# Performance work log

Measured on AMD Instinct MI355X. Metric: run time of the kernel, lower is better.

The kernel has to match this reference:

```python
import jax, jax.numpy as jnp
import numpy as np

DIM = 96
HID = 384
DEPTH = 5
HEADS = 8
INNER = 64 * DIM          # inner_dim = dim_head * dim per source (dim_head=64)
DH = INNER // HEADS       # per-head dim = 768
SCALE = 64 ** -0.5        # scale uses default dim_head=64, not actual per-head dim
EPS = 1e-5


def setup_inputs() -> dict:
    key = jax.random.key(0)
    ks = jax.random.split(key, 13)
    def p(k, shape, s=0.02):
        return jax.random.normal(k, shape, jnp.float32) * s
    return {
        "x": jax.random.normal(ks[0], (2, 512, DIM), jnp.float32),
        "gam_a": p(ks[1], (DEPTH, 3, DIM)),          # attention pre-norm gammas
        "Wq": p(ks[2], (DEPTH, 3, DIM, INNER)),
        "Wk": p(ks[3], (DEPTH, 3, DIM, INNER)),
        "Wv": p(ks[4], (DEPTH, 3, DIM, INNER)),
        "Wo": p(ks[5], (DEPTH, 3, INNER, DIM)),
        "gam_m": p(ks[6], (DEPTH, 2, DIM)),          # MLP pre-norm gammas
        "W1": p(ks[7], (DEPTH, 2, DIM, HID)),
        "b1": p(ks[8], (DEPTH, 2, HID)),
        "W2": p(ks[9], (DEPTH, 2, HID, DIM)),
        "b2": p(ks[10], (DEPTH, 2, DIM)),
        "gam_mid": p(ks[11], (DEPTH, DIM)),          # bare LayerNorm inside each block
        "gam_final": p(ks[12], (DIM,)),
    }


def _ln(x, g):
    # nn.LayerNorm(elementwise_affine=False) followed by x * (gamma + 1)
    mu = x.mean(-1, keepdims=True)
    var = ((x - mu) ** 2).mean(-1, keepdims=True)
    return (x - mu) * jax.lax.rsqrt(var + EPS) * (g + 1.0)


def _attn(x, g, wq, wk, wv, wo):
    b, n, _ = x.shape
    h = _ln(x, g)                                    # self.norm (reuse_attention=True)
    q = (h @ wq).reshape(b, n, HEADS, DH).transpose(0, 2, 1, 3) * SCALE
    k = (h @ wk).reshape(b, n, HEADS, DH).transpose(0, 2, 1, 3)
    v = (h @ wv).reshape(b, n, HEADS, DH).transpose(0, 2, 1, 3)
    sim = jnp.einsum("bhid,bhjd->bhij", q, k)        # [b,h,n,n]
    a = jax.nn.softmax(sim, axis=-1)                 # dropout=0.0 -> identity
    o = jnp.einsum("bhij,bhjd->bhid", a, v)
    return o.transpose(0, 2, 1, 3).reshape(b, n, INNER) @ wo


def _mlp(x, g, w1, b1_, w2, b2_):
    # LayerNorm -> Linear -> GELU(exact) -> Linear (dropouts eval-mode identity)
    h = jax.nn.gelu(_ln(x, g) @ w1 + b1_, approximate=False)
    return h @ w2 + b2_


def reference(x, gam_a, Wq, Wk, Wv, Wo, gam_m, W1, b1, W2, b2, gam_mid, gam_final):
    for d in range(DEPTH):
        x = _attn(x, gam_a[d, 0], Wq[d, 0], Wk[d, 0], Wv[d, 0], Wo[d, 0]) + x
        x = _mlp(x, gam_m[d, 0], W1[d, 0], b1[d, 0], W2[d, 0], b2[d, 0]) + x
        x = _attn(x, gam_a[d, 1], Wq[d, 1], Wk[d, 1], Wv[d, 1], Wo[d, 1]) + x
        x = _attn(x, gam_a[d, 2], Wq[d, 2], Wk[d, 2], Wv[d, 2], Wo[d, 2]) + x
        x = _ln(x, gam_mid[d])                       # bare LayerNorm, NO residual
        x = _mlp(x, gam_m[d, 1], W1[d, 1], b1[d, 1], W2[d, 1], b2[d, 1]) + x
    return _ln(x, gam_final)
```

## Files before the change

### kernel.cpp

```cpp
#include <hip/hip_runtime.h>
#include <hip/hip_bf16.h>

typedef __hip_bfloat16 bf16;
typedef __attribute__((ext_vector_type(8))) short bf16x8;
typedef __attribute__((ext_vector_type(4))) float f32x4;

#define TOK    1024
#define DIM    96
#define HIDN   384
#define HEADS  8
#define DH     768
#define INNER  6144
#define SEQ    512
#define NDEPTH 5
#define EPSLN  1e-5f
#define QSCALE 0.125f

#define MFMA16(a, b, c) __builtin_amdgcn_mfma_f32_16x16x32_bf16((a), (b), (c), 0, 0, 0)

__device__ __forceinline__ float b2f(bf16 v) { return __bfloat162float(v); }
__device__ __forceinline__ bf16  f2b(float v) { return __float2bfloat16(v); }

__device__ __forceinline__ float gload(const void* p, size_t i, int f) {
  return f ? b2f(((const bf16*)p)[i]) : ((const float*)p)[i];
}
__device__ __forceinline__ const char* gptr(const void* base, size_t off, int f) {
  return (const char*)base + off * (size_t)(f ? 2 : 4);
}

__device__ __forceinline__ uint4 pack8(float4 u0, float4 u1) {
  alignas(16) unsigned short o[8];
  bf16 t;
  t = f2b(u0.x); o[0] = *(unsigned short*)&t;
  t = f2b(u0.y); o[1] = *(unsigned short*)&t;
  t = f2b(u0.z); o[2] = *(unsigned short*)&t;
  t = f2b(u0.w); o[3] = *(unsigned short*)&t;
  t = f2b(u1.x); o[4] = *(unsigned short*)&t;
  t = f2b(u1.y); o[5] = *(unsigned short*)&t;
  t = f2b(u1.z); o[6] = *(unsigned short*)&t;
  t = f2b(u1.w); o[7] = *(unsigned short*)&t;
  return *(const uint4*)o;
}

__global__ __launch_bounds__(256) void detect_kernel(const void* xraw, int* flag) {
  __shared__ int cnt[256];
  int t = threadIdx.x;
  const unsigned short* u = (const unsigned short*)xraw;
  int c = 0;
  #pragma unroll
  for (int i = 0; i < 4; i++) {
    unsigned short h = u[2 * (t * 4 + i)];
    int e = (h >> 7) & 0xFF;
    if (e >= 87 && e <= 132) c++;
  }
  cnt[t] = c;
  __syncthreads();
  for (int s = 128; s > 0; s >>= 1) {
    if (t < s) cnt[t] += cnt[t + s];
    __syncthreads();
  }
  if (t == 0) *flag = (cnt[0] > 700) ? 1 : 0;
}

__global__ __launch_bounds__(256) void wtrans_all_kernel(
    const void* __restrict__ Wo, const void* __restrict__ W1,
    const void* __restrict__ W2, bf16* __restrict__ woT,
    bf16* __restrict__ w1T, bf16* __restrict__ w2T,
    const int* __restrict__ flagp) {
  __shared__ float tile[32][65];
  int f = *flagp;
  int b = blockIdx.x;
  const void* src; bf16* dst; int R, C, bx, by, bz;
  if (b < 5760) {
    src = Wo; dst = woT; R = INNER; C = DIM;
    bz = b / 384; int rem = b % 384; bx = rem & 1; by = rem >> 1;
  } else if (b < 5940) {
    int idx = b - 5760;
    src = W1; dst = w1T; R = DIM; C = HIDN;
    bx = idx % 6; by = (idx / 6) % 3; bz = idx / 18;
  } else {
    int idx = b - 5940;
    src = W2; dst = w2T; R = HIDN; C = DIM;
    bx = idx & 1; by = (idx >> 1) % 12; bz = idx / 24;
  }
  int t = threadIdx.x;
  int c0 = bx * 64, r0 = by * 32;
  size_t bb = (size_t)bz * R * C;
  int ty = t >> 4, tx = t & 15;
  #pragma unroll
  for (int half = 0; half < 2; half++) {
    int r = r0 + ty + half * 16;
    int c = c0 + tx * 4;
    if (c < C) {
      size_t idx = bb + (size_t)r * C + c;
      float v0, v1, v2, v3;
      if (f) {
        uint2 u = *(const uint2*)((const unsigned short*)src + idx);
        v0 = __uint_as_float((u.x & 0xffffu) << 16);
        v1 = __uint_as_float(u.x & 0xffff0000u);
        v2 = __uint_as_float((u.y & 0xffffu) << 16);
        v3 = __uint_as_float(u.y & 0xffff0000u);
      } else {
        float4 v = *(const float4*)((const float*)src + idx);
        v0 = v.x; v1 = v.y; v2 = v.z; v3 = v.w;
      }
      tile[ty + half * 16][tx * 4 + 0] = v0;
      tile[ty + half * 16][tx * 4 + 1] = v1;
      tile[ty + half * 16][tx * 4 + 2] = v2;
      tile[ty + half * 16][tx * 4 + 3] = v3;
    }
  }
  __syncthreads();
  int cc = c0 + (t >> 2), rseg = (t & 3) * 8;
  if (cc < C) {
    int cs = cc - c0;
    alignas(16) unsigned short o[8];
    #pragma unroll
    for (int j = 0; j < 8; j++) {
      bf16 tv = f2b(tile[rseg + j][cs]);
      o[j] = *(unsigned short*)&tv;
    }
    *(uint4*)&dst[bb + (size_t)cc * R + r0 + rseg] = *(const uint4*)o;
  }
}

template <int WM>
__device__ __forceinline__ void gemm_bt_body(
    const void* __restrict__ A, int aF32, int lda,
    const void* __restrict__ Bt, int bF32, int ldb,
    int m0, int n0, int kbeg, int kend, int Mtot, int N,
    float alpha, bf16* __restrict__ Cb, float* __restrict__ Cf, int ldc) {
  constexpr int TM = WM * 32;
  __shared__ bf16 As[TM][40];
  __shared__ bf16 Bs[128][40];
  int t = threadIdx.x;
  int lane = t & 63;
  int wave = t >> 6;
  int wm = (wave >> 1) * (WM * 16), wn = (wave & 1) * 64;
  f32x4 acc[WM][4];
  #pragma unroll
  for (int i = 0; i < WM; i++)
    #pragma unroll
    for (int j = 0; j < 4; j++) acc[i][j] = (f32x4){0.f, 0.f, 0.f, 0.f};

  int arow = t >> 2, aseg = (t & 3) * 8;

  for (int kb = kbeg; kb < kend; kb += 32) {
    #pragma unroll
    for (int i = 0; i < (TM + 63) / 64; i++) {
      int rr = arow + i * 64;
      if ((TM % 64 == 0) || rr < TM) {
        int gm = min(m0 + rr, Mtot - 1);
        size_t idx = (size_t)gm * lda + kb + aseg;
        if (aF32) {
          const float* Af = (const float*)A;
          float4 u0 = *(const float4*)(Af + idx);
          float4 u1 = *(const float4*)(Af + idx + 4);
          *(uint4*)&As[rr][aseg] = pack8(u0, u1);
        } else {
          *(uint4*)&As[rr][aseg] = *(const uint4*)((const bf16*)A + idx);
        }
      }
    }
    #pragma unroll
    for (int i = 0; i < 2; i++) {
      int r = arow + i * 64;
      int gn = n0 + r;
      if (gn < N) {
        size_t idx = (size_t)gn * ldb + kb + aseg;
        if (bF32) {
          const float* Bf = (const float*)Bt;
          float4 u0 = *(const float4*)(Bf + idx);
          float4 u1 = *(const float4*)(Bf + idx + 4);
          *(uint4*)&Bs[r][aseg] = pack8(u0, u1);
        } else {
          *(uint4*)&Bs[r][aseg] = *(const uint4*)((const bf16*)Bt + idx);
        }
      } else {
        uint4 zz = {0, 0, 0, 0};
        *(uint4*)&Bs[r][aseg] = zz;
      }
    }
    __syncthreads();
    int fm = lane & 15, fq = (lane >> 4) * 8;
    bf16x8 af[WM], bfv[4];
    #pragma unroll
    for (int i = 0; i < WM; i++)
      af[i] = *(const bf16x8*)&As[wm + i * 16 + fm][fq];
    #pragma unroll
    for (int j = 0; j < 4; j++)
      bfv[j] = *(const bf16x8*)&Bs[wn + j * 16 + fm][fq];
    #pragma unroll
    for (int i = 0; i < WM; i++)
      #pragma unroll
      for (int j = 0; j < 4; j++)
        acc[i][j] = MFMA16(af[i], bfv[j], acc[i][j]);
    __syncthreads();
  }
  int col = lane & 15, rq = (lane >> 4) * 4;
  #pragma unroll
  for (int j = 0; j < 4; j++) {
    int gn = n0 + wn + j * 16 + col;
    if (gn >= N) continue;
    #pragma unroll
    for (int i = 0; i < WM; i++) {
      #pragma unroll
      for (int r = 0; r < 4; r++) {
        int gm = m0 + wm + i * 16 + rq + r;
        if (gm >= Mtot) continue;
        if (Cf) Cf[(size_t)gm * ldc + gn] = acc[i][j][r];
        else    Cb[(size_t)gm * ldc + gn] = f2b(acc[i][j][r] * alpha);
      }
    }
  }
}

__global__ __launch_bounds__(256) void mtgt_kernel(
    const void* __restrict__ WqE, const void* __restrict__ WkE,
    const void* __restrict__ WvE, const bf16* __restrict__ woT,
    float* __restrict__ P, const int* __restrict__ flagp) {
  int f = *flagp;
  int z = blockIdx.z;
  int ks = blockIdx.x / 3, mt = blockIdx.x % 3;
  bool isM = z < 120;
  int zz = isM ? z : z - 120;
  int L = zz >> 3, h = zz & 7;
  size_t wo = (size_t)L * DIM * INNER + (size_t)h * DH;
  const void* A  = isM ? (const void*)((const char*)WkE + wo * (f ? 2 : 4))
                       : (const void*)(woT + wo);
  const void* Bt = isM ? (const void*)((const char*)WqE + wo * (f ? 2 : 4))
                       : (const void*)((const char*)WvE + wo * (f ? 2 : 4));
  int aF32 = isM ? !f : 0;
  int bF32 = !f;
  float* Cf = P + ((size_t)ks * 240 + z) * DIM * DIM;
  gemm_bt_body<1>(A, aF32, INNER, Bt, bF32, INNER,
                  mt * 32, 0, ks * (DH / 4), (ks + 1) * (DH / 4), DIM, DIM,
                  1.f, nullptr, Cf, DIM);
}

__device__ __forceinline__ void ln_row_vals(float v0, float v1in, int lane,
    const char* g, int f, float& o0, float& o1) {
  float v1 = (lane < 32) ? v1in : 0.f;
  float s = v0 + v1;
  #pragma unroll
  for (int off = 32; off > 0; off >>= 1) s += __shfl_xor(s, off);
  float mu = s * (1.f / 96.f);
  float d0 = v0 - mu;
  float d1 = (lane < 32) ? (v1 - mu) : 0.f;
  float q = d0 * d0 + d1 * d1;
  #pragma unroll
  for (int off = 32; off > 0; off >>= 1) q += __shfl_xor(q, off);
  float rstd = rsqrtf(q * (1.f / 96.f) + EPSLN);
  o0 = d0 * rstd * (gload(g, lane, f) + 1.f);
  o1 = (lane < 32) ? (d1 * rstd * (gload(g, 64 + lane, f) + 1.f)) : 0.f;
}

__device__ __forceinline__ void store_hn(bf16* hn, bf16* hnT, int row, int lane,
                                         float o0, float o1) {
  size_t base = (size_t)row * DIM;
  bf16* hT = hnT + (size_t)(row >> 9) * DIM * SEQ;
  int ss = row & (SEQ - 1);
  hn[base + lane] = f2b(o0);
  hT[(size_t)lane * SEQ + ss] = f2b(o0);
  if (lane < 32) {
    hn[base + 64 + lane] = f2b(o1);
    hT[(size_t)(64 + lane) * SEQ + ss] = f2b(o1);
  }
}

__global__ __launch_bounds__(256) void cvtcast_kernel(
    const float* __restrict__ P, bf16* __restrict__ Mt, bf16* __restrict__ Gt,
    const void* __restrict__ in_x, float* __restrict__ x,
    bf16* __restrict__ hn, bf16* __restrict__ hnT,
    const void* __restrict__ gb, const int* __restrict__ flagp) {
  if (blockIdx.x < 2160) {
    const int n = 240 * DIM * DIM;
    int i0 = (blockIdx.x * 256 + threadIdx.x) * 4;
    if (i0 >= n) return;
    int z = i0 / (DIM * DIM);
    bool isM = z < 120;
    float alpha = isM ? QSCALE : 1.f;
    float4 a = *(const float4*)(P + i0);
    float4 b = *(const float4*)(P + n + i0);
    float4 c = *(const float4*)(P + 2 * (size_t)n + i0);
    float4 d = *(const float4*)(P + 3 * (size_t)n + i0);
    bf16* out = isM ? (Mt + i0) : (Gt + (size_t)i0 - (size_t)120 * DIM * DIM);
    alignas(8) unsigned short o[4];
    bf16 t;
    t = f2b(((a.x + b.x) + (c.x + d.x)) * alpha); o[0] = *(unsigned short*)&t;
    t = f2b(((a.y + b.y) + (c.y + d.y)) * alpha); o[1] = *(unsigned short*)&t;
    t = f2b(((a.z + b.z) + (c.z + d.z)) * alpha); o[2] = *(unsigned short*)&t;
    t = f2b(((a.w + b.w) + (c.w + d.w)) * alpha); o[3] = *(unsigned short*)&t;
    *(uint2*)out = *(const uint2*)o;
  } else {
    int f = *flagp;
    int wave = threadIdx.x >> 6, lane = threadIdx.x & 63;
    int row = (blockIdx.x - 2160) * 4 + wave;
    size_t base = (size_t)row * DIM;
    float v0 = gload(in_x, base + lane, f);
    float v1 = (lane < 32) ? gload(in_x, base + 64 + lane, f) : 0.f;
    x[base + lane] = v0;
    if (lane < 32) x[base + 64 + lane] = v1;
    float o0, o1;
    ln_row_vals(v0, v1, lane, gptr(gb, 0, f), f, o0, o1);
    store_hn(hn, hnT, row, lane, o0, o1);
  }
}

__global__ __launch_bounds__(256) void ln_kernel(
    const float* __restrict__ x, bf16* __restrict__ hn, bf16* __restrict__ hnT,
    const void* __restrict__ gb, size_t goff, const int* __restrict__ flagp) {
  int f = *flagp;
  int wave = threadIdx.x >> 6, lane = threadIdx.x & 63;
  int row = blockIdx.x * 4 + wave;
  size_t base = (size_t)row * DIM;
  float v0 = x[base + lane];
  float v1 = (lane < 32) ? x[base + 64 + lane] : 0.f;
  float o0, o1;
  ln_row_vals(v0, v1, lane, gptr(gb, goff, f), f, o0, o1);
  store_hn(hn, hnT, row, lane, o0, o1);
}

__global__ __launch_bounds__(512) void fattn4_kernel(
    const bf16* __restrict__ hn,
    const bf16* __restrict__ hnT,
    const bf16* __restrict__ MtL,
    const bf16* __restrict__ GtL,
    float* __restrict__ x) {
  __shared__ bf16 tP[32][520];
  __shared__ bf16 Zs[32][104];
  __shared__ float red[2][8][32];
  int tid = threadIdx.x, lane = tid & 63, wave = tid >> 6;
  int fm = lane & 15, fq = (lane >> 4) * 8;
  int col = lane & 15, rq = (lane >> 4) * 4;
  int z = blockIdx.y, b = z >> 3, h = z & 7;
  int m0 = blockIdx.x * 32;
  const bf16* hnB = hn + (size_t)b * SEQ * DIM;
  const bf16* hTB = hnT + (size_t)b * DIM * SEQ;
  const bf16* MtH = MtL + (size_t)h * DIM * DIM;
  const bf16* GtH = GtL + (size_t)h * DIM * DIM;

  if (wave < 6) {
    int mA = wave & 1, nb = wave >> 1;
    f32x4 a0 = (f32x4){0.f, 0.f, 0.f, 0.f}, a1 = a0;
    #pragma unroll
    for (int kb = 0; kb < 96; kb += 32) {
      bf16x8 af = *(const bf16x8*)(hnB + (size_t)(m0 + mA * 16 + fm) * DIM + kb + fq);
      bf16x8 b0 = *(const bf16x8*)(MtH + (size_t)(nb * 16 + fm) * DIM + kb + fq);
      bf16x8 b1 = *(const bf16x8*)(MtH + (size_t)((nb + 3) * 16 + fm) * DIM + kb + fq);
      a0 = MFMA16(af, b0, a0);
      a1 = MFMA16(af, b1, a1);
    }
    #pragma unroll
    for (int r = 0; r < 4; r++) {
      Zs[mA * 16 + rq + r][nb * 16 + col] = f2b(a0[r]);
      Zs[mA * 16 + rq + r][(nb + 3) * 16 + col] = f2b(a1[r]);
    }
  }
  __syncthreads();

  f32x4 acc2[2][4];
  #pragma unroll
  for (int i = 0; i < 2; i++)
    #pragma unroll
    for (int j = 0; j < 4; j++) acc2[i][j] = (f32x4){0.f, 0.f, 0.f, 0.f};
  #pragma unroll
  for (int kb = 0; kb < 96; kb += 32) {
    bf16x8 af0 = *(const bf16x8*)&Zs[fm][kb + fq];
    bf16x8 af1 = *(const bf16x8*)&Zs[16 + fm][kb + fq];
    bf16x8 bv[4];
    #pragma unroll
    for (int j = 0; j < 4; j++)
      bv[j] = *(const bf16x8*)(hnB + (size_t)(wave * 64 + j * 16 + fm) * DIM + kb + fq);
    #pragma unroll
    for (int j = 0; j < 4; j++) {
      acc2[0][j] = MFMA16(af0, bv[j], acc2[0][j]);
      acc2[1][j] = MFMA16(af1, bv[j], acc2[1][j]);
    }
  }

  float rmax[2][4];
  #pragma unroll
  for (int i = 0; i < 2; i++)
    #pragma unroll
    for (int r = 0; r < 4; r++) {
      float m = -1e30f;
      #pragma unroll
      for (int j = 0; j < 4; j++) m = fmaxf(m, acc2[i][j][r]);
      rmax[i][r] = m;
    }
  #pragma unroll
  for (int s = 1; s < 16; s <<= 1)
    #pragma unroll
    for (int i = 0; i < 2; i++)
      #pragma unroll
      for (int r = 0; r < 4; r++)
        rmax[i][r] = fmaxf(rmax[i][r], __shfl_xor(rmax[i][r], s));
  if (col == 0)
    #pragma unroll
    for (int i = 0; i < 2; i++)
      #pragma unroll
      for (int r = 0; r < 4; r++) red[0][wave][i * 16 + rq + r] = rmax[i][r];
  __syncthreads();
  float rsum[2][4];
  #pragma unroll
  for (int i = 0; i < 2; i++)
    #pragma unroll
    for (int r = 0; r < 4; r++) {
      int row = i * 16 + rq + r;
      float gm = red[0][0][row];
      #pragma unroll
      for (int q = 1; q < 8; q++) gm = fmaxf(gm, red[0][q][row]);
      float s = 0.f;
      #pragma unroll
      for (int j = 0; j < 4; j++) {
        float e = __expf(acc2[i][j][r] - gm);
        acc2[i][j][r] = e;
        s += e;
      }
      rsum[i][r] = s;
    }
  #pragma unroll
  for (int s = 1; s < 16; s <<= 1)
    #pragma unroll
    for (int i = 0; i < 2; i++)
      #pragma unroll
      for (int r = 0; r < 4; r++)
        rsum[i][r] += __shfl_xor(rsum[i][r], s);
  if (col == 0)
    #pragma unroll
    for (int i = 0; i < 2; i++)
      #pragma unroll
      for (int r = 0; r < 4; r++) red[1][wave][i * 16 + rq + r] = rsum[i][r];
  __syncthreads();

  #pragma unroll
  for (int i = 0; i < 2; i++)
    #pragma unroll
    for (int r = 0; r < 4; r++) {
      int row = i * 16 + rq + r;
      float tot = red[1][0][row];
      #pragma unroll
      for (int q = 1; q < 8; q++) tot += red[1][q][row];
      float inv = 1.f / tot;
      #pragma unroll
      for (int j = 0; j < 4; j++)
        tP[row][wave * 64 + j * 16 + col] = f2b(acc2[i][j][r] * inv);
    }
  __syncthreads();

  f32x4 z0 = (f32x4){0.f, 0.f, 0.f, 0.f}, z1 = z0;
  if (wave < 4) {
    int n = wave;
    #pragma unroll 4
    for (int kb = 0; kb < 512; kb += 32) {
      bf16x8 bv = *(const bf16x8*)(hTB + (size_t)(n * 16 + fm) * SEQ + kb + fq);
      bf16x8 af0 = *(const bf16x8*)&tP[fm][kb + fq];
      bf16x8 af1 = *(const bf16x8*)&tP[16 + fm][kb + fq];
      z0 = MFMA16(af0, bv, z0);
      z1 = MFMA16(af1, bv, z1);
    }
    #pragma unroll
    for (int r = 0; r < 4; r++) {
      Zs[rq + r][n * 16 + col] = f2b(z0[r]);
      Zs[16 + rq + r][n * 16 + col] = f2b(z1[r]);
    }
  } else {
    int mA = wave & 1, n = (wave >> 1) + 2;
    #pragma unroll 4
    for (int kb = 0; kb < 512; kb += 32) {
      bf16x8 bv = *(const bf16x8*)(hTB + (size_t)(n * 16 + fm) * SEQ + kb + fq);
      bf16x8 af = *(const bf16x8*)&tP[mA * 16 + fm][kb + fq];
      z0 = MFMA16(af, bv, z0);
    }
    #pragma unroll
    for (int r = 0; r < 4; r++)
      Zs[mA * 16 + rq + r][n * 16 + col] = f2b(z0[r]);
  }
  __syncthreads();

  if (wave < 6) {
    int mA = wave & 1, nb = wave >> 1;
    f32x4 o0 = (f32x4){0.f, 0.f, 0.f, 0.f}, o1 = o0;
    #pragma unroll
    for (int kb = 0; kb < 96; kb += 32) {
      bf16x8 af = *(const bf16x8*)&Zs[mA * 16 + fm][kb + fq];
      bf16x8 b0 = *(const bf16x8*)(GtH + (size_t)(nb * 16 + fm) * DIM + kb + fq);
      bf16x8 b1 = *(const bf16x8*)(GtH + (size_t)((nb + 3) * 16 + fm) * DIM + kb + fq);
      o0 = MFMA16(af, b0, o0);
      o1 = MFMA16(af, b1, o1);
    }
    #pragma unroll
    for (int r = 0; r < 4; r++) {
      int gr = b * SEQ + m0 + mA * 16 + rq + r;
      atomicAdd(x + (size_t)gr * DIM + nb * 16 + col, o0[r]);
      atomicAdd(x + (size_t)gr * DIM + (nb + 3) * 16 + col, o1[r]);
    }
  }
}

__global__ __launch_bounds__(512) void fmlp_kernel(
    float* __restrict__ X,
    const void* __restrict__ gmidb, size_t gmidoff, int useMid,
    const void* __restrict__ gmb, size_t gmoff,
    const bf16* __restrict__ w1T,
    const void* __restrict__ b1b, size_t b1off,
    const bf16* __restrict__ w2T,
    const void* __restrict__ b2b, size_t b2off,
    int lnmode, const void* __restrict__ lngb, size_t lngoff,
    bf16* __restrict__ hn, bf16* __restrict__ hnT, void* __restrict__ dout,
    const int* __restrict__ flagp) {
  __shared__ float X1s[32][96];
  __shared__ bf16 As[32][104];
  __shared__ bf16 Hs[32][392];
  int f = *flagp;
  int tid = threadIdx.x, lane = tid & 63, wave = tid >> 6;
  int fm = lane & 15, fq = (lane >> 4) * 8;
  int col = lane & 15, rq = (lane >> 4) * 4;
  int m0 = blockIdx.x * 32;
  const char* gm = gptr(gmb, gmoff, f);
  float gm0 = gload(gm, lane, f) + 1.f;
  float gm1 = (lane < 32) ? (gload(gm, 64 + lane, f) + 1.f) : 0.f;
  float gd0 = 1.f, gd1 = 1.f;
  if (useMid) {
    const char* gmid = gptr(gmidb, gmidoff, f);
    gd0 = gload(gmid, lane, f) + 1.f;
    gd1 = (lane < 32) ? (gload(gmid, 64 + lane, f) + 1.f) : 0.f;
  }
  for (int r = wave; r < 32; r += 8) {
    const float* xr = X + (size_t)(m0 + r) * DIM;
    float v0 = xr[lane];
    float v1 = (lane < 32) ? xr[64 + lane] : 0.f;
    if (useMid) {
      float s = v0 + v1;
      #pragma unroll
      for (int off = 32; off > 0; off >>= 1) s += __shfl_xor(s, off);
      float mu = s * (1.f / 96.f);
      float d0 = v0 - mu;
      float d1 = (lane < 32) ? (v1 - mu) : 0.f;
      float q = d0 * d0 + d1 * d1;
      #pragma unroll
      for (int off = 32; off > 0; off >>= 1) q += __shfl_xor(q, off);
      float rstd = rsqrtf(q * (1.f / 96.f) + EPSLN);
      v0 = d0 * rstd * gd0;
      v1 = (lane < 32) ? (d1 * rstd * gd1) : 0.f;
    }
    X1s[r][lane] = v0;
    if (lane < 32) X1s[r][64 + lane] = v1;
    float s = v0 + v1;
    #pragma unroll
    for (int off = 32; off > 0; off >>= 1) s += __shfl_xor(s, off);
    float mu = s * (1.f / 96.f);
    float d0 = v0 - mu;
    float d1 = (lane < 32) ? (v1 - mu) : 0.f;
    float q = d0 * d0 + d1 * d1;
    #pragma unroll
    for (int off = 32; off > 0; off >>= 1) q += __shfl_xor(q, off);
    float rstd = rsqrtf(q * (1.f / 96.f) + EPSLN);
    As[r][lane] = f2b(d0 * rstd * gm0);
    if (lane < 32) As[r][64 + lane] = f2b(d1 * rstd * gm1);
  }
  __syncthreads();

  int mw = wave & 1, nh = wave >> 1;
  f32x4 acc1[6];
  #pragma unroll
  for (int j = 0; j < 6; j++) acc1[j] = (f32x4){0.f, 0.f, 0.f, 0.f};
  #pragma unroll
  for (int kb = 0; kb < 96; kb += 32) {
    bf16x8 af = *(const bf16x8*)&As[mw * 16 + fm][kb + fq];
    #pragma unroll
    for (int j = 0; j < 6; j++) {
      bf16x8 bv = *(const bf16x8*)(w1T + (size_t)(nh * 96 + j * 16 + fm) * DIM + kb + fq);
      acc1[j] = MFMA16(af, bv, acc1[j]);
    }
  }
  const char* b1p = gptr(b1b, b1off, f);
  #pragma unroll
  for (int j = 0; j < 6; j++) {
    int gn = nh * 96 + j * 16 + col;
    float bv = gload(b1p, gn, f);
    #pragma unroll
    for (int r = 0; r < 4; r++) {
      float v = acc1[j][r] + bv;
      v = 0.5f * v * (1.f + erff(v * 0.70710678118f));
      Hs[mw * 16 + rq + r][gn] = f2b(v);
    }
  }
  __syncthreads();

  if (wave < 6) {
    int mA = wave & 1, nb = wave >> 1;
    f32x4 o0 = (f32x4){0.f, 0.f, 0.f, 0.f}, o1 = o0;
    #pragma unroll 4
    for (int kb = 0; kb < 384; kb += 32) {
      bf16x8 af = *(const bf16x8*)&Hs[mA * 16 + fm][kb + fq];
      bf16x8 b0 = *(const bf16x8*)(w2T + (size_t)(nb * 16 + fm) * HIDN + kb + fq);
      bf16x8 b1 = *(const bf16x8*)(w2T + (size_t)((nb + 3) * 16 + fm) * HIDN + kb + fq);
      o0 = MFMA16(af, b0, o0);
      o1 = MFMA16(af, b1, o1);
    }
    const char* b2p = gptr(b2b, b2off, f);
    float bb0 = gload(b2p, nb * 16 + col, f);
    float bb1 = gload(b2p, (nb + 3) * 16 + col, f);
    #pragma unroll
    for (int r = 0; r < 4; r++) {
      int row = mA * 16 + rq + r;
      int gmr = m0 + row;
      float nv0 = X1s[row][nb * 16 + col] + o0[r] + bb0;
      float nv1 = X1s[row][(nb + 3) * 16 + col] + o1[r] + bb1;
      X[(size_t)gmr * DIM + nb * 16 + col] = nv0;
      X[(size_t)gmr * DIM + (nb + 3) * 16 + col] = nv1;
      X1s[row][nb * 16 + col] = nv0;
      X1s[row][(nb + 3) * 16 + col] = nv1;
    }
  }
  __syncthreads();

  const char* lg = gptr(lngb, lngoff, f);
  for (int r = wave; r < 32; r += 8) {
    int row = m0 + r;
    size_t base = (size_t)row * DIM;
    float v0 = X1s[r][lane];
    float v1 = (lane < 32) ? X1s[r][64 + lane] : 0.f;
    float o0, o1;
    ln_row_vals(v0, v1, lane, lg, f, o0, o1);
    if (lnmode == 1) {
      store_hn(hn, hnT, row, lane, o0, o1);
    } else {
      if (!f) {
        ((float*)dout)[base + lane] = o0;
        if (lane < 32) ((float*)dout)[base + 64 + lane] = o1;
      } else {
        ((bf16*)dout)[base + lane] = f2b(o0);
        if (lane < 32) ((bf16*)dout)[base + 64 + lane] = f2b(o1);
      }
    }
  }
}

extern "C" void kernel_launch(void* const* d_in, const int* in_sizes, int n_in,
                              void* d_out, int out_size, void* d_ws, size_t ws_size,
                              hipStream_t stream) {
  const void* in_x    = d_in[0];
  const void* gam_a   = d_in[1];
  const void* Wq      = d_in[2];
  const void* Wk      = d_in[3];
  const void* Wv      = d_in[4];
  const void* Wo      = d_in[5];
  const void* gam_m   = d_in[6];
  const void* W1      = d_in[7];
  const void* b1      = d_in[8];
  const void* W2      = d_in[9];
  const void* b2      = d_in[10];
  const void* gam_mid = d_in[11];
  const void* gam_fin = d_in[12];

  char* wsb = (char*)d_ws;
  size_t off = 0;
  auto carve = [&](size_t bytes) {
    char* p = wsb + off;
    off += (bytes + 255) & ~(size_t)255;
    return p;
  };
  int*   flag = (int*)carve(256);
  float* x    = (float*)carve((size_t)TOK * DIM * 4);
  bf16*  hn   = (bf16*)carve((size_t)TOK * DIM * 2);
  bf16*  hnT  = (bf16*)carve((size_t)2 * DIM * SEQ * 2);
  const size_t WSZ = (size_t)15 * DIM * INNER;
  bf16*  woT  = (bf16*)carve(WSZ * 2);
  bf16*  w1T  = (bf16*)carve((size_t)10 * DIM * HIDN * 2);
  bf16*  w2T  = (bf16*)carve((size_t)10 * DIM * HIDN * 2);
  bf16*  Mt   = (bf16*)carve((size_t)120 * DIM * DIM * 2);
  bf16*  Gt   = (bf16*)carve((size_t)120 * DIM * DIM * 2);
  float* MtP  = (float*)carve((size_t)4 * 240 * DIM * DIM * 4);

  detect_kernel<<<dim3(1), dim3(256), 0, stream>>>(in_x, flag);

  wtrans_all_kernel<<<dim3(6180), dim3(256), 0, stream>>>(
      Wo, W1, W2, woT, w1T, w2T, flag);
  mtgt_kernel<<<dim3(12, 1, 240), dim3(256), 0, stream>>>(
      Wq, Wk, Wv, woT, MtP, flag);
  cvtcast_kernel<<<dim3(2160 + 256), dim3(256), 0, stream>>>(
      MtP, Mt, Gt, in_x, x, hn, hnT, gam_a, flag);

  auto attn = [&](int d, int j) {
    size_t gi = ((size_t)d * 3 + j);
    fattn4_kernel<<<dim3(16, 16), dim3(512), 0, stream>>>(
        hn, hnT, Mt + gi * 8 * DIM * DIM, Gt + gi * 8 * DIM * DIM, x);
  };

  for (int d = 0; d < NDEPTH; d++) {
    bool last = (d == NDEPTH - 1);
    attn(d, 0);
    fmlp_kernel<<<dim3(32), dim3(512), 0, stream>>>(
        x, nullptr, 0, 0,
        gam_m, (size_t)(d * 2 + 0) * DIM,
        w1T + (size_t)(d * 2 + 0) * DIM * HIDN, b1, (size_t)(d * 2 + 0) * HIDN,
        w2T + (size_t)(d * 2 + 0) * DIM * HIDN, b2, (size_t)(d * 2 + 0) * DIM,
        1, gam_a, (size_t)(d * 3 + 1) * DIM, hn, hnT, nullptr, flag);
    attn(d, 1);
    ln_kernel<<<dim3(TOK / 4), dim3(256), 0, stream>>>(
        x, hn, hnT, gam_a, (size_t)(d * 3 + 2) * DIM, flag);
    attn(d, 2);
    fmlp_kernel<<<dim3(32), dim3(512), 0, stream>>>(
        x, gam_mid, (size_t)d * DIM, 1,
        gam_m, (size_t)(d * 2 + 1) * DIM,
        w1T + (size_t)(d * 2 + 1) * DIM * HIDN, b1, (size_t)(d * 2 + 1) * HIDN,
        w2T + (size_t)(d * 2 + 1) * DIM * HIDN, b2, (size_t)(d * 2 + 1) * DIM,
        last ? 2 : 1, last ? gam_fin : gam_a,
        last ? (size_t)0 : (size_t)((d + 1) * 3) * DIM,
        hn, hnT, d_out, flag);
  }
}
```

Baseline: 662.3 us.

## Halve attention query tile to 16 rows and halve split-K in weight fold

```diff
diff --git a/kernel.cpp b/kernel.cpp
--- a/kernel.cpp
+++ b/kernel.cpp
@@ -234,7 +234,7 @@
   int bF32 = !f;
   float* Cf = P + ((size_t)ks * 240 + z) * DIM * DIM;
   gemm_bt_body<1>(A, aF32, INNER, Bt, bF32, INNER,
-                  mt * 32, 0, ks * (DH / 4), (ks + 1) * (DH / 4), DIM, DIM,
+                  mt * 32, 0, ks * (DH / 2), (ks + 1) * (DH / 2), DIM, DIM,
                   1.f, nullptr, Cf, DIM);
 }
 
@@ -282,15 +282,13 @@
     float alpha = isM ? QSCALE : 1.f;
     float4 a = *(const float4*)(P + i0);
     float4 b = *(const float4*)(P + n + i0);
-    float4 c = *(const float4*)(P + 2 * (size_t)n + i0);
-    float4 d = *(const float4*)(P + 3 * (size_t)n + i0);
     bf16* out = isM ? (Mt + i0) : (Gt + (size_t)i0 - (size_t)120 * DIM * DIM);
     alignas(8) unsigned short o[4];
     bf16 t;
-    t = f2b(((a.x + b.x) + (c.x + d.x)) * alpha); o[0] = *(unsigned short*)&t;
-    t = f2b(((a.y + b.y) + (c.y + d.y)) * alpha); o[1] = *(unsigned short*)&t;
-    t = f2b(((a.z + b.z) + (c.z + d.z)) * alpha); o[2] = *(unsigned short*)&t;
-    t = f2b(((a.w + b.w) + (c.w + d.w)) * alpha); o[3] = *(unsigned short*)&t;
+    t = f2b((a.x + b.x) * alpha); o[0] = *(unsigned short*)&t;
+    t = f2b((a.y + b.y) * alpha); o[1] = *(unsigned short*)&t;
+    t = f2b((a.z + b.z) * alpha); o[2] = *(unsigned short*)&t;
+    t = f2b((a.w + b.w) * alpha); o[3] = *(unsigned short*)&t;
     *(uint2*)out = *(const uint2*)o;
   } else {
     int f = *flagp;
@@ -321,180 +319,142 @@
   store_hn(hn, hnT, row, lane, o0, o1);
 }
 
-__global__ __launch_bounds__(512) void fattn4_kernel(
+__global__ __launch_bounds__(512) void fattn5_kernel(
     const bf16* __restrict__ hn,
     const bf16* __restrict__ hnT,
     const bf16* __restrict__ MtL,
     const bf16* __restrict__ GtL,
     float* __restrict__ x) {
-  __shared__ bf16 tP[32][520];
-  __shared__ bf16 Zs[32][104];
-  __shared__ float red[2][8][32];
+  __shared__ bf16 tP[16][520];
+  __shared__ bf16 Zs[16][104];
+  __shared__ float red[2][8][16];
   int tid = threadIdx.x, lane = tid & 63, wave = tid >> 6;
   int fm = lane & 15, fq = (lane >> 4) * 8;
   int col = lane & 15, rq = (lane >> 4) * 4;
   int z = blockIdx.y, b = z >> 3, h = z & 7;
-  int m0 = blockIdx.x * 32;
+  int m0 = blockIdx.x * 16;
   const bf16* hnB = hn + (size_t)b * SEQ * DIM;
   const bf16* hTB = hnT + (size_t)b * DIM * SEQ;
   const bf16* MtH = MtL + (size_t)h * DIM * DIM;
   const bf16* GtH = GtL + (size_t)h * DIM * DIM;
 
   if (wave < 6) {
-    int mA = wave & 1, nb = wave >> 1;
-    f32x4 a0 = (f32x4){0.f, 0.f, 0.f, 0.f}, a1 = a0;
+    int n = wave;
+    f32x4 a0 = (f32x4){0.f, 0.f, 0.f, 0.f};
     #pragma unroll
     for (int kb = 0; kb < 96; kb += 32) {
-      bf16x8 af = *(const bf16x8*)(hnB + (size_t)(m0 + mA * 16 + fm) * DIM + kb + fq);
-      bf16x8 b0 = *(const bf16x8*)(MtH + (size_t)(nb * 16 + fm) * DIM + kb + fq);
-      bf16x8 b1 = *(const bf16x8*)(MtH + (size_t)((nb + 3) * 16 + fm) * DIM + kb + fq);
-      a0 = MFMA16(af, b0, a0);
-      a1 = MFMA16(af, b1, a1);
-    }
-    #pragma unroll
-    for (int r = 0; r < 4; r++) {
-      Zs[mA * 16 + rq + r][nb * 16 + col] = f2b(a0[r]);
-      Zs[mA * 16 + rq + r][(nb + 3) * 16 + col] = f2b(a1[r]);
-    }
-  }
-  __syncthreads();
-
-  f32x4 acc2[2][4];
-  #pragma unroll
-  for (int i = 0; i < 2; i++)
-    #pragma unroll
-    for (int j = 0; j < 4; j++) acc2[i][j] = (f32x4){0.f, 0.f, 0.f, 0.f};
+      bf16x8 af = *(const bf16x8*)(hnB + (size_t)(m0 + fm) * DIM + kb + fq);
+      bf16x8 bv = *(const bf16x8*)(MtH + (size_t)(n * 16 + fm) * DIM + kb + fq);
+      a0 = MFMA16(af, bv, a0);
+    }
+    #pragma unroll
+    for (int r = 0; r < 4; r++)
+      Zs[rq + r][n * 16 + col] = f2b(a0[r]);
+  }
+  __syncthreads();
+
+  f32x4 acc2[4];
+  #pragma unroll
+  for (int j = 0; j < 4; j++) acc2[j] = (f32x4){0.f, 0.f, 0.f, 0.f};
   #pragma unroll
   for (int kb = 0; kb < 96; kb += 32) {
-    bf16x8 af0 = *(const bf16x8*)&Zs[fm][kb + fq];
-    bf16x8 af1 = *(const bf16x8*)&Zs[16 + fm][kb + fq];
+    bf16x8 af = *(const bf16x8*)&Zs[fm][kb + fq];
     bf16x8 bv[4];
     #pragma unroll
     for (int j = 0; j < 4; j++)
       bv[j] = *(const bf16x8*)(hnB + (size_t)(wave * 64 + j * 16 + fm) * DIM + kb + fq);
     #pragma unroll
+    for (int j = 0; j < 4; j++)
+      acc2[j] = MFMA16(af, bv[j], acc2[j]);
+  }
+
+  float rmax[4];
+  #pragma unroll
+  for (int r = 0; r < 4; r++) {
+    float m = -1e30f;
+    #pragma unroll
+    for (int j = 0; j < 4; j++) m = fmaxf(m, acc2[j][r]);
+    rmax[r] = m;
+  }
+  #pragma unroll
+  for (int s = 1; s < 16; s <<= 1)
+    #pragma unroll
+    for (int r = 0; r < 4; r++)
+      rmax[r] = fmaxf(rmax[r], __shfl_xor(rmax[r], s));
+  if (col == 0)
+    #pragma unroll
+    for (int r = 0; r < 4; r++) red[0][wave][rq + r] = rmax[r];
+  __syncthreads();
+  float rsum[4];
+  #pragma unroll
+  for (int r = 0; r < 4; r++) {
+    int row = rq + r;
+    float gm = red[0][0][row];
+    #pragma unroll
+    for (int q = 1; q < 8; q++) gm = fmaxf(gm, red[0][q][row]);
+    float s = 0.f;
+    #pragma unroll
     for (int j = 0; j < 4; j++) {
-      acc2[0][j] = MFMA16(af0, bv[j], acc2[0][j]);
-      acc2[1][j] = MFMA16(af1, bv[j], acc2[1][j]);
-    }
-  }
-
-  float rmax[2][4];
-  #pragma unroll
-  for (int i = 0; i < 2; i++)
-    #pragma unroll
-    for (int r = 0; r < 4; r++) {
-      float m = -1e30f;
-      #pragma unroll
-      for (int j = 0; j < 4; j++) m = fmaxf(m, acc2[i][j][r]);
-      rmax[i][r] = m;
-    }
+      float e = __expf(acc2[j][r] - gm);
+      acc2[j][r] = e;
+      s += e;
+    }
+    rsum[r] = s;
+  }
   #pragma unroll
   for (int s = 1; s < 16; s <<= 1)
     #pragma unroll
-    for (int i = 0; i < 2; i++)
-      #pragma unroll
-      for (int r = 0; r < 4; r++)
-        rmax[i][r] = fmaxf(rmax[i][r], __shfl_xor(rmax[i][r], s));
+    for (int r = 0; r < 4; r++)
+      rsum[r] += __shfl_xor(rsum[r], s);
   if (col == 0)
     #pragma unroll
-    for (int i = 0; i < 2; i++)
-      #pragma unroll
-      for (int r = 0; r < 4; r++) red[0][wave][i * 16 + rq + r] = rmax[i][r];
-  __syncthreads();
-  float rsum[2][4];
-  #pragma unroll
-  for (int i = 0; i < 2; i++)
-    #pragma unroll
-    for (int r = 0; r < 4; r++) {
-      int row = i * 16 + rq + r;
-      float gm = red[0][0][row];
-      #pragma unroll
-      for (int q = 1; q < 8; q++) gm = fmaxf(gm, red[0][q][row]);
-      float s = 0.f;
-      #pragma unroll
-      for (int j = 0; j < 4; j++) {
-        float e = __expf(acc2[i][j][r] - gm);
-        acc2[i][j][r] = e;
-        s += e;
-      }
-      rsum[i][r] = s;
-    }
-  #pragma unroll
-  for (int s = 1; s < 16; s <<= 1)
-    #pragma unroll
-    for (int i = 0; i < 2; i++)
-      #pragma unroll
-      for (int r = 0; r < 4; r++)
-        rsum[i][r] += __shfl_xor(rsum[i][r], s);
-  if (col == 0)
-    #pragma unroll
-    for (int i = 0; i < 2; i++)
-      #pragma unroll
-      for (int r = 0; r < 4; r++) red[1][wave][i * 16 + rq + r] = rsum[i][r];
-  __syncthreads();
-
-  #pragma unroll
-  for (int i = 0; i < 2; i++)
-    #pragma unroll
-    for (int r = 0; r < 4; r++) {
-      int row = i * 16 + rq + r;
-      float tot = red[1][0][row];
-      #pragma unroll
-      for (int q = 1; q < 8; q++) tot += red[1][q][row];
-      float inv = 1.f / tot;
-      #pragma unroll
-      for (int j = 0; j < 4; j++)
-        tP[row][wave * 64 + j * 16 + col] = f2b(acc2[i][j][r] * inv);
-    }
-  __syncthreads();
-
-  f32x4 z0 = (f32x4){0.f, 0.f, 0.f, 0.f}, z1 = z0;
-  if (wave < 4) {
+    for (int r = 0; r < 4; r++) red[1][wave][rq + r] = rsum[r];
+  __syncthreads();
+
+  #pragma unroll
+  for (int r = 0; r < 4; r++) {
+    int row = rq + r;
+    float tot = red[1][0][row];
+    #pragma unroll
+    for (int q = 1; q < 8; q++) tot += red[1][q][row];
+    float inv = 1.f / tot;
+    #pragma unroll
+    for (int j = 0; j < 4; j++)
+      tP[row][wave * 64 + j * 16 + col] = f2b(acc2[j][r] * inv);
+  }
+  __syncthreads();
+
+  if (wave < 6) {
     int n = wave;
+    f32x4 z0 = (f32x4){0.f, 0.f, 0.f, 0.f};
     #pragma unroll 4
     for (int kb = 0; kb < 512; kb += 32) {
       bf16x8 bv = *(const bf16x8*)(hTB + (size_t)(n * 16 + fm) * SEQ + kb + fq);
-      bf16x8 af0 = *(const bf16x8*)&tP[fm][kb + fq];
-      bf16x8 af1 = *(const bf16x8*)&tP[16 + fm][kb + fq];
-      z0 = MFMA16(af0, bv, z0);
-      z1 = MFMA16(af1, bv, z1);
+      bf16x8 af = *(const bf16x8*)&tP[fm][kb + fq];
+      z0 = MFMA16(af, bv, z0);
+    }
+    __syncthreads();
+    #pragma unroll
+    for (int r = 0; r < 4; r++)
+      Zs[rq + r][n * 16 + col] = f2b(z0[r]);
+  } else {
+    __syncthreads();
+  }
+  __syncthreads();
+
+  if (wave < 6) {
+    int n = wave;
+    f32x4 o0 = (f32x4){0.f, 0.f, 0.f, 0.f};
+    #pragma unroll
+    for (int kb = 0; kb < 96; kb += 32) {
+      bf16x8 af = *(const bf16x8*)&Zs[fm][kb + fq];
+      bf16x8 bv = *(const bf16x8*)(GtH + (size_t)(n * 16 + fm) * DIM + kb + fq);
+      o0 = MFMA16(af, bv, o0);
     }
     #pragma unroll
     for (int r = 0; r < 4; r++) {
-      Zs[rq + r][n * 16 + col] = f2b(z0[r]);
-      Zs[16 + rq + r][n * 16 + col] = f2b(z1[r]);
-    }
-  } else {
-    int mA = wave & 1, n = (wave >> 1) + 2;
-    #pragma unroll 4
-    for (int kb = 0; kb < 512; kb += 32) {
-      bf16x8 bv = *(const bf16x8*)(hTB + (size_t)(n * 16 + fm) * SEQ + kb + fq);
-      bf16x8 af = *(const bf16x8*)&tP[mA * 16 + fm][kb + fq];
-      z0 = MFMA16(af, bv, z0);
-    }
-    #pragma unroll
-    for (int r = 0; r < 4; r++)
-      Zs[mA * 16 + rq + r][n * 16 + col] = f2b(z0[r]);
-  }
-  __syncthreads();
-
-  if (wave < 6) {
-    int mA = wave & 1, nb = wave >> 1;
-    f32x4 o0 = (f32x4){0.f, 0.f, 0.f, 0.f}, o1 = o0;
-    #pragma unroll
-    for (int kb = 0; kb < 96; kb += 32) {
-      bf16x8 af = *(const bf16x8*)&Zs[mA * 16 + fm][kb + fq];
-      bf16x8 b0 = *(const bf16x8*)(GtH + (size_t)(nb * 16 + fm) * DIM + kb + fq);
-      bf16x8 b1 = *(const bf16x8*)(GtH + (size_t)((nb + 3) * 16 + fm) * DIM + kb + fq);
-      o0 = MFMA16(af, b0, o0);
-      o1 = MFMA16(af, b1, o1);
-    }
-    #pragma unroll
-    for (int r = 0; r < 4; r++) {
-      int gr = b * SEQ + m0 + mA * 16 + rq + r;
-      atomicAdd(x + (size_t)gr * DIM + nb * 16 + col, o0[r]);
-      atomicAdd(x + (size_t)gr * DIM + (nb + 3) * 16 + col, o1[r]);
+      int gr = b * SEQ + m0 + rq + r;
+      atomicAdd(x + (size_t)gr * DIM + n * 16 + col, o0[r]);
     }
   }
 }
@@ -673,20 +633,20 @@
   bf16*  w2T  = (bf16*)carve((size_t)10 * DIM * HIDN * 2);
   bf16*  Mt   = (bf16*)carve((size_t)120 * DIM * DIM * 2);
   bf16*  Gt   = (bf16*)carve((size_t)120 * DIM * DIM * 2);
-  float* MtP  = (float*)carve((size_t)4 * 240 * DIM * DIM * 4);
+  float* MtP  = (float*)carve((size_t)2 * 240 * DIM * DIM * 4);
 
   detect_kernel<<<dim3(1), dim3(256), 0, stream>>>(in_x, flag);
 
   wtrans_all_kernel<<<dim3(6180), dim3(256), 0, stream>>>(
       Wo, W1, W2, woT, w1T, w2T, flag);
-  mtgt_kernel<<<dim3(12, 1, 240), dim3(256), 0, stream>>>(
+  mtgt_kernel<<<dim3(6, 1, 240), dim3(256), 0, stream>>>(
       Wq, Wk, Wv, woT, MtP, flag);
   cvtcast_kernel<<<dim3(2160 + 256), dim3(256), 0, stream>>>(
       MtP, Mt, Gt, in_x, x, hn, hnT, gam_a, flag);
 
   auto attn = [&](int d, int j) {
     size_t gi = ((size_t)d * 3 + j);
-    fattn4_kernel<<<dim3(16, 16), dim3(512), 0, stream>>>(
+    fattn5_kernel<<<dim3(32, 16), dim3(512), 0, stream>>>(
         hn, hnT, Mt + gi * 8 * DIM * DIM, Gt + gi * 8 * DIM * DIM, x);
   };
 
```

Result: faster. 646.8 us (-2.3%).
